# Kernel optimization log

Hardware: AMD Instinct MI355X
Metric: run time of the kernel (lower is better)

Reference implementation:

```python
import jax, jax.numpy as jnp
import numpy as np

B, S, D, H = 4, 2048, 1024, 16
Dh = D // H


def _layernorm(x, a, b):
    # torch.var default is unbiased (ddof=1)
    mu = jnp.mean(x, axis=-1, keepdims=True)
    sg = jnp.var(x, axis=-1, keepdims=True, ddof=1)
    return (x - mu) / jnp.sqrt(sg + 1e-08) * a + b


def setup_inputs() -> dict:
    key = jax.random.key(0)
    ks = jax.random.split(key, 16)
    s = 1.0 / np.sqrt(D)
    inp = {
        'q': jax.random.normal(ks[0], (B, S, D), jnp.float32),
        'k': jax.random.normal(ks[1], (B, S, D), jnp.float32),
        'v': jax.random.normal(ks[2], (B, S, D), jnp.float32),
        'g': jax.random.normal(ks[3], (B, S, D), jnp.float32),
        # causal mask: True = masked
        'm': jnp.triu(jnp.ones((S, S), jnp.bool_), k=1)[None, None],
        'Wq': jax.random.uniform(ks[4], (D, D), jnp.float32, -s, s),
        'bq': jnp.zeros((D,), jnp.float32),
        'Wk': jax.random.uniform(ks[5], (D, D), jnp.float32, -s, s),
        'bk': jnp.zeros((D,), jnp.float32),
        'Wv': jax.random.uniform(ks[6], (D, D), jnp.float32, -s, s),
        'bv': jnp.zeros((D,), jnp.float32),
        'Wg': jax.random.uniform(ks[7], (D, D), jnp.float32, -s, s),
        'bg': jnp.zeros((D,), jnp.float32),
        'ln_a': jnp.ones((D,), jnp.float32),
        'ln_b': jnp.zeros((D,), jnp.float32),
        'Wo': jax.random.uniform(ks[8], (D, D), jnp.float32, -s, s),
        'bo': jnp.zeros((D,), jnp.float32),
    }
    return inp


def reference(q, k, v, g, m, Wq, bq, Wk, bk, Wv, bv, Wg, bg, ln_a, ln_b, Wo, bo):
    qp = q @ Wq.T + bq
    kp = k @ Wk.T + bk
    vp = v @ Wv.T + bv
    gp = g @ Wg.T + bg
    # gating path: exact GELU (torch default), then custom LayerNorm (unbiased var)
    vp = jax.nn.gelu(vp, approximate=False)
    gp = jax.nn.gelu(gp, approximate=False)
    vp = _layernorm(vp, ln_a, ln_b)
    # [B,S,D] -> [B,H,S,Dh]
    qh = qp.reshape(B, S, H, Dh).transpose(0, 2, 1, 3)
    kh = kp.reshape(B, S, H, Dh).transpose(0, 2, 1, 3)
    vh = vp.reshape(B, S, H, Dh).transpose(0, 2, 1, 3)
    gh = gp.reshape(B, S, H, Dh).transpose(0, 2, 1, 3)
    a = jnp.einsum('bhqd,bhkd->bhqk', qh, kh) / jnp.sqrt(jnp.float32(Dh))
    a = jnp.where(m, -jnp.inf, a)
    a = jax.nn.softmax(a, axis=-1)
    # dropout = 0.0 (inference): no-op
    o = jnp.einsum('bhqk,bhkd->bhqd', a, vh)
    o = o * gh
    o = o.transpose(0, 2, 1, 3).reshape(B, S, D)
    o = o @ Wo.T + bo
    return (o, a)
```

## Files before the change

### kernel.cpp

```cpp
#include <hip/hip_runtime.h>
#include <hip/hip_bf16.h>
#include <cstdint>
#include <cstddef>

#define DEVINL static __device__ __forceinline__

typedef short bf16x8 __attribute__((ext_vector_type(8)));
typedef short s16x4  __attribute__((ext_vector_type(4)));
typedef float f32x4  __attribute__((ext_vector_type(4)));
typedef unsigned short u16;

static constexpr int Bb = 4, Ss = 2048, Dd = 1024, Hh = 16;
static constexpr int Mrows = Bb * Ss;
static constexpr int BHc = Bb * Hh;

DEVINL u16 f2bf(float f) {
    union { float f; uint32_t u; } v; v.f = f;
    uint32_t r = v.u + 0x7fffu + ((v.u >> 16) & 1u);
    return (u16)(r >> 16);
}
DEVINL float bf2f(u16 h) {
    union { uint32_t u; float f; } v; v.u = ((uint32_t)h) << 16;
    return v.f;
}
DEVINL uint32_t cvt_pk_bf16(float lo, float hi) {
    uint32_t r;
    asm("v_cvt_pk_bf16_f32 %0, %1, %2" : "=v"(r) : "v"(lo), "v"(hi));
    return r;
}
DEVINL float gelu_exact(float x) {
    return 0.5f * x * (1.0f + erff(x * 0.70710678118654752f));
}
DEVINL void gload16(const u16* gsrc, u16* ldsdst) {
    auto* g = reinterpret_cast<const __attribute__((address_space(1))) uint32_t*>(
        reinterpret_cast<uintptr_t>(gsrc));
    auto* l = reinterpret_cast<__attribute__((address_space(3))) uint32_t*>(
        reinterpret_cast<uintptr_t>(ldsdst));
    __builtin_amdgcn_global_load_lds(g, l, 16, 0, 0);
}

__global__ __launch_bounds__(256) void k_cvt_in(
    const float* __restrict__ s0, const float* __restrict__ s1,
    const float* __restrict__ s2, const float* __restrict__ s3,
    u16* __restrict__ d0, u16* __restrict__ d1,
    u16* __restrict__ d2, u16* __restrict__ d3, int n4) {
    int t = blockIdx.x * 256 + threadIdx.x;
    if (t >= n4) return;
    const float* s; u16* d;
    switch (blockIdx.y) {
        case 0: s = s0; d = d0; break;
        case 1: s = s1; d = d1; break;
        case 2: s = s2; d = d2; break;
        default: s = s3; d = d3; break;
    }
    float4 v = ((const float4*)s)[t];
    ushort4 o;
    o.x = f2bf(v.x); o.y = f2bf(v.y); o.z = f2bf(v.z); o.w = f2bf(v.w);
    ((ushort4*)d)[t] = o;
}

__global__ __launch_bounds__(256) void k_cvt_w(
    const float* __restrict__ s0, const float* __restrict__ s1,
    const float* __restrict__ s2, const float* __restrict__ s3,
    const float* __restrict__ s4,
    u16* __restrict__ d0, u16* __restrict__ d1, u16* __restrict__ d2,
    u16* __restrict__ d3, u16* __restrict__ d4, int n4) {
    int t = blockIdx.x * 256 + threadIdx.x;
    if (t >= n4) return;
    const float* s; u16* d;
    switch (blockIdx.y) {
        case 0: s = s0; d = d0; break;
        case 1: s = s1; d = d1; break;
        case 2: s = s2; d = d2; break;
        case 3: s = s3; d = d3; break;
        default: s = s4; d = d4; break;
    }
    float4 v = ((const float4*)s)[t];
    ushort4 o;
    o.x = f2bf(v.x); o.y = f2bf(v.y); o.z = f2bf(v.z); o.w = f2bf(v.w);
    ((ushort4*)d)[t] = o;
}

__global__ __launch_bounds__(256, 3) void k_proj(
    const u16* __restrict__ qb, const u16* __restrict__ kb,
    const u16* __restrict__ vb, const u16* __restrict__ gb,
    const u16* __restrict__ Wqb, const u16* __restrict__ Wkb,
    const u16* __restrict__ Wvb, const u16* __restrict__ Wgb,
    const float* __restrict__ bqp, const float* __restrict__ bkp,
    const float* __restrict__ bvp, const float* __restrict__ bgp,
    u16* __restrict__ qp, u16* __restrict__ kpo,
    float* __restrict__ vp, u16* __restrict__ ghb)
{
    __shared__ u16 As[2][128 * 32];
    __shared__ u16 Bs[2][128 * 32];
    const int tid = threadIdx.x, lane = tid & 63, w = tid >> 6;
    const int wm = w >> 1, wn = w & 1;
    const int g = lane >> 4, li = lane & 15;
    const int orig = blockIdx.x;
    const int lid = (orig & 7) * 256 + (orig >> 3);
    const int z = lid >> 9, rem = lid & 511;
    const int m0 = (rem >> 3) * 128, n0 = (rem & 7) * 128;

    const u16 *Ap, *Wp; const float* bias;
    switch (z) {
        case 0: Ap = qb; Wp = Wqb; bias = bqp; break;
        case 1: Ap = kb; Wp = Wkb; bias = bkp; break;
        case 2: Ap = vb; Wp = Wvb; bias = bvp; break;
        default: Ap = gb; Wp = Wgb; bias = bgp; break;
    }

    const int ch0 = (w * 2 + 0) * 64 + lane, ch1 = (w * 2 + 1) * 64 + lane;
    const int row0 = ch0 >> 2, cp0 = ch0 & 3, row1 = ch1 >> 2, cp1 = ch1 & 3;
    const size_t aoff0 = (size_t)(m0 + row0) * 1024 + ((cp0 ^ ((row0 >> 1) & 3)) << 3);
    const size_t aoff1 = (size_t)(m0 + row1) * 1024 + ((cp1 ^ ((row1 >> 1) & 3)) << 3);
    const size_t boff0 = (size_t)(n0 + row0) * 1024 + ((cp0 ^ ((row0 >> 1) & 3)) << 3);
    const size_t boff1 = (size_t)(n0 + row1) * 1024 + ((cp1 ^ ((row1 >> 1) & 3)) << 3);
    const int ldst0 = (w * 2 + 0) * 512, ldst1 = (w * 2 + 1) * 512;

    const f32x4 zero4 = {0.f, 0.f, 0.f, 0.f};
    f32x4 acc[4][4];
#pragma unroll
    for (int m = 0; m < 4; m++)
#pragma unroll
        for (int n = 0; n < 4; n++) acc[m][n] = zero4;

    gload16(Ap + aoff0,      &As[0][ldst0]);
    gload16(Ap + aoff1,      &As[0][ldst1]);
    gload16(Wp + boff0,      &Bs[0][ldst0]);
    gload16(Wp + boff1,      &Bs[0][ldst1]);
    gload16(Ap + aoff0 + 32, &As[1][ldst0]);
    gload16(Ap + aoff1 + 32, &As[1][ldst1]);
    gload16(Wp + boff0 + 32, &Bs[1][ldst0]);
    gload16(Wp + boff1 + 32, &Bs[1][ldst1]);
    asm volatile("s_waitcnt vmcnt(4)" ::: "memory");
    asm volatile("s_barrier" ::: "memory");

    for (int kt = 0; kt < 32; ++kt) {
        const int cur = kt & 1;
        bf16x8 af[4], bfr[4];
#pragma unroll
        for (int m = 0; m < 4; m++) {
            int row = wm * 64 + m * 16 + li;
            af[m] = *(const bf16x8*)&As[cur][row * 32 + ((g ^ ((row >> 1) & 3)) << 3)];
        }
#pragma unroll
        for (int n = 0; n < 4; n++) {
            int row = wn * 64 + n * 16 + li;
            bfr[n] = *(const bf16x8*)&Bs[cur][row * 32 + ((g ^ ((row >> 1) & 3)) << 3)];
        }
#pragma unroll
        for (int m = 0; m < 4; m++)
#pragma unroll
            for (int n = 0; n < 4; n++)
                acc[m][n] = __builtin_amdgcn_mfma_f32_16x16x32_bf16(af[m], bfr[n], acc[m][n], 0, 0, 0);
        asm volatile("s_barrier" ::: "memory");
        if (kt + 2 < 32) {
            const int k0n = (kt + 2) * 32;
            gload16(Ap + aoff0 + k0n, &As[cur][ldst0]);
            gload16(Ap + aoff1 + k0n, &As[cur][ldst1]);
            gload16(Wp + boff0 + k0n, &Bs[cur][ldst0]);
            gload16(Wp + boff1 + k0n, &Bs[cur][ldst1]);
            asm volatile("s_waitcnt vmcnt(4)" ::: "memory");
        } else {
            asm volatile("s_waitcnt vmcnt(0)" ::: "memory");
        }
        asm volatile("s_barrier" ::: "memory");
    }

#pragma unroll
    for (int m = 0; m < 4; m++) {
#pragma unroll
        for (int n = 0; n < 4; n++) {
            int col = n0 + wn * 64 + n * 16 + li;
            float bv = bias[col];
#pragma unroll
            for (int r = 0; r < 4; r++) {
                int row = m0 + wm * 64 + m * 16 + g * 4 + r;
                float v = acc[m][n][r] + bv;
                size_t idx = (size_t)row * 1024 + col;
                if (z == 0)      qp[idx]  = f2bf(v * 0.125f);
                else if (z == 1) kpo[idx] = f2bf(v);
                else if (z == 2) vp[idx]  = gelu_exact(v);
                else             ghb[idx] = f2bf(gelu_exact(v));
            }
        }
    }
}

__global__ __launch_bounds__(256, 3) void k_gemm_f(
    const u16* __restrict__ Ap, const u16* __restrict__ Wp,
    const float* __restrict__ bias, float* __restrict__ Cp)
{
    __shared__ u16 As[2][128 * 32];
    __shared__ u16 Bs[2][128 * 32];
    const int tid = threadIdx.x, lane = tid & 63, w = tid >> 6;
    const int wm = w >> 1, wn = w & 1;
    const int g = lane >> 4, li = lane & 15;
    const int orig = blockIdx.x;
    const int lid = (orig & 7) * 64 + (orig >> 3);
    const int m0 = (lid >> 3) * 128, n0 = (lid & 7) * 128;

    const int ch0 = (w * 2 + 0) * 64 + lane, ch1 = (w * 2 + 1) * 64 + lane;
    const int row0 = ch0 >> 2, cp0 = ch0 & 3, row1 = ch1 >> 2, cp1 = ch1 & 3;
    const size_t aoff0 = (size_t)(m0 + row0) * 1024 + ((cp0 ^ ((row0 >> 1) & 3)) << 3);
    const size_t aoff1 = (size_t)(m0 + row1) * 1024 + ((cp1 ^ ((row1 >> 1) & 3)) << 3);
    const size_t boff0 = (size_t)(n0 + row0) * 1024 + ((cp0 ^ ((row0 >> 1) & 3)) << 3);
    const size_t boff1 = (size_t)(n0 + row1) * 1024 + ((cp1 ^ ((row1 >> 1) & 3)) << 3);
    const int ldst0 = (w * 2 + 0) * 512, ldst1 = (w * 2 + 1) * 512;

    const f32x4 zero4 = {0.f, 0.f, 0.f, 0.f};
    f32x4 acc[4][4];
#pragma unroll
    for (int m = 0; m < 4; m++)
#pragma unroll
        for (int n = 0; n < 4; n++) acc[m][n] = zero4;

    gload16(Ap + aoff0,      &As[0][ldst0]);
    gload16(Ap + aoff1,      &As[0][ldst1]);
    gload16(Wp + boff0,      &Bs[0][ldst0]);
    gload16(Wp + boff1,      &Bs[0][ldst1]);
    gload16(Ap + aoff0 + 32, &As[1][ldst0]);
    gload16(Ap + aoff1 + 32, &As[1][ldst1]);
    gload16(Wp + boff0 + 32, &Bs[1][ldst0]);
    gload16(Wp + boff1 + 32, &Bs[1][ldst1]);
    asm volatile("s_waitcnt vmcnt(4)" ::: "memory");
    asm volatile("s_barrier" ::: "memory");

    for (int kt = 0; kt < 32; ++kt) {
        const int cur = kt & 1;
        bf16x8 af[4], bfr[4];
#pragma unroll
        for (int m = 0; m < 4; m++) {
            int row = wm * 64 + m * 16 + li;
            af[m] = *(const bf16x8*)&As[cur][row * 32 + ((g ^ ((row >> 1) & 3)) << 3)];
        }
#pragma unroll
        for (int n = 0; n < 4; n++) {
            int row = wn * 64 + n * 16 + li;
            bfr[n] = *(const bf16x8*)&Bs[cur][row * 32 + ((g ^ ((row >> 1) & 3)) << 3)];
        }
#pragma unroll
        for (int m = 0; m < 4; m++)
#pragma unroll
            for (int n = 0; n < 4; n++)
                acc[m][n] = __builtin_amdgcn_mfma_f32_16x16x32_bf16(af[m], bfr[n], acc[m][n], 0, 0, 0);
        asm volatile("s_barrier" ::: "memory");
        if (kt + 2 < 32) {
            const int k0n = (kt + 2) * 32;
            gload16(Ap + aoff0 + k0n, &As[cur][ldst0]);
            gload16(Ap + aoff1 + k0n, &As[cur][ldst1]);
            gload16(Wp + boff0 + k0n, &Bs[cur][ldst0]);
            gload16(Wp + boff1 + k0n, &Bs[cur][ldst1]);
            asm volatile("s_waitcnt vmcnt(4)" ::: "memory");
        } else {
            asm volatile("s_waitcnt vmcnt(0)" ::: "memory");
        }
        asm volatile("s_barrier" ::: "memory");
    }

#pragma unroll
    for (int m = 0; m < 4; m++) {
#pragma unroll
        for (int n = 0; n < 4; n++) {
            int col = n0 + wn * 64 + n * 16 + li;
            float bv = bias[col];
#pragma unroll
            for (int r = 0; r < 4; r++) {
                int row = m0 + wm * 64 + m * 16 + g * 4 + r;
                Cp[(size_t)row * 1024 + col] = acc[m][n][r] + bv;
            }
        }
    }
}

__global__ __launch_bounds__(256) void k_ln(const float* __restrict__ vp,
                                            const float* __restrict__ la,
                                            const float* __restrict__ lb,
                                            u16* __restrict__ vh) {
    int row = blockIdx.x;
    const float* x = vp + (size_t)row * 1024;
    int tid = threadIdx.x;
    float4 v = ((const float4*)x)[tid];
    float s = v.x + v.y + v.z + v.w;
    float s2 = v.x * v.x + v.y * v.y + v.z * v.z + v.w * v.w;
#pragma unroll
    for (int off = 1; off < 64; off <<= 1) {
        s  += __shfl_xor(s, off, 64);
        s2 += __shfl_xor(s2, off, 64);
    }
    __shared__ float red[8];
    int w = tid >> 6, lane = tid & 63;
    if (lane == 0) { red[w] = s; red[4 + w] = s2; }
    __syncthreads();
    s  = red[0] + red[1] + red[2] + red[3];
    s2 = red[4] + red[5] + red[6] + red[7];
    float mu = s * (1.0f / 1024.0f);
    float var = (s2 - 1024.0f * mu * mu) * (1.0f / 1023.0f);
    float rs = rsqrtf(var + 1e-8f);
    float4 a4 = ((const float4*)la)[tid];
    float4 b4 = ((const float4*)lb)[tid];
    ushort4 o;
    o.x = f2bf((v.x - mu) * rs * a4.x + b4.x);
    o.y = f2bf((v.y - mu) * rs * a4.y + b4.y);
    o.z = f2bf((v.z - mu) * rs * a4.z + b4.z);
    o.w = f2bf((v.w - mu) * rs * a4.w + b4.w);
    ((ushort4*)(vh + (size_t)row * 1024))[tid] = o;
}

__global__ __launch_bounds__(256) void k_transpose(const u16* __restrict__ vh,
                                                   u16* __restrict__ vhT) {
    int bh = blockIdx.y, b = bh >> 4, h = bh & 15, s0 = blockIdx.x * 64;
    __shared__ u16 t[64 * 96];
    int tid = threadIdx.x;
#pragma unroll
    for (int j = 0; j < 2; j++) {
        int u = j * 256 + tid;
        int r = u >> 3, c8 = u & 7;
        bf16x8 v = *(const bf16x8*)(vh + ((size_t)(b * 2048 + s0 + r) * 1024 + h * 64 + c8 * 8));
        *(bf16x8*)&t[r * 96 + c8 * 8] = v;
    }
    __syncthreads();
#pragma unroll
    for (int j = 0; j < 2; j++) {
        int u = j * 256 + tid;
        int d = u >> 3, s8 = u & 7;
        bf16x8 vv;
#pragma unroll
        for (int jj = 0; jj < 8; jj++) vv[jj] = (short)t[(s8 * 8 + jj) * 96 + d];
        *(bf16x8*)(vhT + ((size_t)(bh * 64 + d) * 2048 + s0 + s8 * 8)) = vv;
    }
}

__global__ __launch_bounds__(512) void k_attn(const u16* __restrict__ qp,
                                              const u16* __restrict__ kp,
                                              const u16* __restrict__ vhT,
                                              const u16* __restrict__ gh,
                                              float* __restrict__ aout,
                                              u16* __restrict__ gated) {
    __shared__ short Ps[8 * 16 * 128];
    const int tid = threadIdx.x, lane = tid & 63, w = tid >> 6;
    const int g = lane >> 4, li = lane & 15;
    const int orig = blockIdx.x;
    const int lid = (orig & 7) * 64 + (orig >> 3);
    const int bh = lid >> 3, i0 = lid & 7;
    const int b = bh >> 4, h = bh & 15;
    const u16* kbh = kp + ((size_t)(b * 2048) * 1024 + h * 64);
    const u16* vbh = vhT + (size_t)bh * 64 * 2048;
    const u16* ghb_base = gh + (size_t)(b * 2048) * 1024 + h * 64;
    float* arow = aout + (size_t)bh * 2048 * 2048;
    short* Pw = &Ps[w * 2048];
    const f32x4 zero4 = {0.f, 0.f, 0.f, 0.f};

    for (int half = 0; half < 2; ++half) {
        const int bx = half ? (15 - i0) : i0;
        const int q0 = bx * 128;
        const int qrow0 = q0 + w * 16;
        const int qrow = qrow0 + li;
        const u16* qbase = qp + ((size_t)(b * 2048 + qrow) * 1024 + h * 64 + g * 8);
        bf16x8 qa0 = *(const bf16x8*)qbase;
        bf16x8 qa1 = *(const bf16x8*)(qbase + 32);

        for (int kt = bx + 1; kt < 16; ++kt) {
            float* tbase = arow + (size_t)q0 * 2048 + kt * 128;
#pragma unroll
            for (int i = 0; i < 8; i++) {
                int u = i * 512 + tid;
                int row = u >> 5, cu = u & 31;
                __builtin_nontemporal_store(zero4, (f32x4*)(tbase + (size_t)row * 2048 + cu * 4));
            }
        }

        float l_run = 0.f;
        for (int kt = 0; kt <= bx; ++kt) {
            const int k0 = kt * 128;
            const bool full = (kt < bx);
#pragma unroll
            for (int n = 0; n < 8; n++) {
                int rb = k0 + n * 16 + li;
                const u16* krow = kbh + (size_t)rb * 1024 + g * 8;
                bf16x8 kb0 = *(const bf16x8*)krow;
                bf16x8 kb1 = *(const bf16x8*)(krow + 32);
                f32x4 c = zero4;
                c = __builtin_amdgcn_mfma_f32_16x16x32_bf16(kb0, qa0, c, 0, 0, 0);
                c = __builtin_amdgcn_mfma_f32_16x16x32_bf16(kb1, qa1, c, 0, 0, 0);
                if (full) {
#pragma unroll
                    for (int r = 0; r < 4; r++) l_run += __expf(c[r]);
                } else {
#pragma unroll
                    for (int r = 0; r < 4; r++) {
                        int col = k0 + n * 16 + g * 4 + r;
                        l_run += (col <= qrow) ? __expf(c[r]) : 0.0f;
                    }
                }
            }
        }
        l_run += __shfl_xor(l_run, 16, 64);
        l_run += __shfl_xor(l_run, 32, 64);
        const float linv = 1.0f / l_run;

        f32x4 oacc[4];
#pragma unroll
        for (int n = 0; n < 4; n++) oacc[n] = zero4;
        for (int kt = 0; kt <= bx; ++kt) {
            const int k0 = kt * 128;
            const bool full = (kt < bx);
#pragma unroll
            for (int n = 0; n < 8; n++) {
                int rb = k0 + n * 16 + li;
                const u16* krow = kbh + (size_t)rb * 1024 + g * 8;
                bf16x8 kb0 = *(const bf16x8*)krow;
                bf16x8 kb1 = *(const bf16x8*)(krow + 32);
                f32x4 c = zero4;
                c = __builtin_amdgcn_mfma_f32_16x16x32_bf16(kb0, qa0, c, 0, 0, 0);
                c = __builtin_amdgcn_mfma_f32_16x16x32_bf16(kb1, qa1, c, 0, 0, 0);
                if (full) {
#pragma unroll
                    for (int r = 0; r < 4; r++) c[r] = __expf(c[r]) * linv;
                } else {
#pragma unroll
                    for (int r = 0; r < 4; r++) {
                        int col = k0 + n * 16 + g * 4 + r;
                        c[r] = (col <= qrow) ? __expf(c[r]) * linv : 0.0f;
                    }
                }
                __builtin_nontemporal_store(c,
                    (f32x4*)(arow + (size_t)qrow * 2048 + k0 + n * 16 + g * 4));
                uint2 pk;
                pk.x = cvt_pk_bf16(c[0], c[1]);
                pk.y = cvt_pk_bf16(c[2], c[3]);
                int chunk = n * 2 + (g >> 1);
                *(uint2*)&Pw[li * 128 + ((chunk ^ (li & 7)) << 3) + (g & 1) * 4] = pk;
            }
#pragma unroll
            for (int ks = 0; ks < 4; ++ks) {
                int cl = ks * 4 + g;
                bf16x8 pa = *(const bf16x8*)&Pw[li * 128 + ((cl ^ (li & 7)) << 3)];
#pragma unroll
                for (int n = 0; n < 4; n++) {
                    int vr = n * 16 + li;
                    bf16x8 vb = *(const bf16x8*)(vbh + (size_t)vr * 2048 + k0 + cl * 8);
                    oacc[n] = __builtin_amdgcn_mfma_f32_16x16x32_bf16(pa, vb, oacc[n], 0, 0, 0);
                }
            }
        }

#pragma unroll
        for (int n = 0; n < 4; n++) {
            int d8 = n * 2 + (li >> 3), wi = li & 7;
#pragma unroll
            for (int r = 0; r < 4; r++) {
                int lr = g * 4 + r;
                Pw[lr * 64 + ((d8 ^ (lr & 7)) << 3) + wi] = (short)f2bf(oacc[n][r]);
            }
        }
#pragma unroll
        for (int it = 0; it < 2; ++it) {
            int lr = it * 8 + (lane >> 3);
            int c8 = lane & 7;
            int rowq = qrow0 + lr;
            bf16x8 ov = *(const bf16x8*)&Pw[lr * 64 + ((c8 ^ (lr & 7)) << 3)];
            bf16x8 gv = *(const bf16x8*)(ghb_base + (size_t)rowq * 1024 + c8 * 8);
            float p0 = bf2f((u16)ov[0]) * bf2f((u16)gv[0]);
            float p1 = bf2f((u16)ov[1]) * bf2f((u16)gv[1]);
            float p2 = bf2f((u16)ov[2]) * bf2f((u16)gv[2]);
            float p3 = bf2f((u16)ov[3]) * bf2f((u16)gv[3]);
            float p4 = bf2f((u16)ov[4]) * bf2f((u16)gv[4]);
            float p5 = bf2f((u16)ov[5]) * bf2f((u16)gv[5]);
            float p6 = bf2f((u16)ov[6]) * bf2f((u16)gv[6]);
            float p7 = bf2f((u16)ov[7]) * bf2f((u16)gv[7]);
            uint4 outv;
            outv.x = cvt_pk_bf16(p0, p1);
            outv.y = cvt_pk_bf16(p2, p3);
            outv.z = cvt_pk_bf16(p4, p5);
            outv.w = cvt_pk_bf16(p6, p7);
            *(uint4*)(gated + ((size_t)(b * 2048 + rowq)) * 1024 + h * 64 + c8 * 8) = outv;
        }
    }
}

extern "C" void kernel_launch(void* const* d_in, const int* in_sizes, int n_in,
                              void* d_out, int out_size, void* d_ws, size_t ws_size,
                              hipStream_t stream) {
    const float* q  = (const float*)d_in[0];
    const float* k  = (const float*)d_in[1];
    const float* v  = (const float*)d_in[2];
    const float* g  = (const float*)d_in[3];
    const float* Wq = (const float*)d_in[5];
    const float* bq = (const float*)d_in[6];
    const float* Wk = (const float*)d_in[7];
    const float* bk = (const float*)d_in[8];
    const float* Wv = (const float*)d_in[9];
    const float* bv = (const float*)d_in[10];
    const float* Wg = (const float*)d_in[11];
    const float* bg = (const float*)d_in[12];
    const float* ln_a = (const float*)d_in[13];
    const float* ln_b = (const float*)d_in[14];
    const float* Wo = (const float*)d_in[15];
    const float* bo = (const float*)d_in[16];

    float* o_out = (float*)d_out;
    float* a_out = o_out + (size_t)Mrows * Dd;

    u16* qp    = (u16*)d_ws;
    u16* kpb   = qp    + (size_t)Mrows * Dd;
    u16* vhT   = kpb   + (size_t)Mrows * Dd;
    u16* ghb   = vhT   + (size_t)Mrows * Dd;
    u16* gated = ghb   + (size_t)Mrows * Dd;
    u16* Wo_bf = gated + (size_t)Mrows * Dd;

    u16* Wq_bf = (u16*)a_out;
    u16* Wk_bf = Wq_bf + (size_t)Dd * Dd;
    u16* Wv_bf = Wk_bf + (size_t)Dd * Dd;
    u16* Wg_bf = Wv_bf + (size_t)Dd * Dd;
    u16* qb    = Wg_bf + (size_t)Dd * Dd;
    u16* kb2   = qb    + (size_t)Mrows * Dd;
    u16* vb    = kb2   + (size_t)Mrows * Dd;
    u16* gb    = vb    + (size_t)Mrows * Dd;
    float* vp  = (float*)(gb + (size_t)Mrows * Dd);
    u16* vh    = (u16*)(vp + (size_t)Mrows * Dd);

    {
        int n4w = Dd * Dd / 4;
        dim3 gw((n4w + 255) / 256, 5);
        k_cvt_w<<<gw, 256, 0, stream>>>(Wq, Wk, Wv, Wg, Wo,
                                        Wq_bf, Wk_bf, Wv_bf, Wg_bf, Wo_bf, n4w);
        int n4i = Mrows * Dd / 4;
        dim3 gi((n4i + 255) / 256, 4);
        k_cvt_in<<<gi, 256, 0, stream>>>(q, k, v, g, qb, kb2, vb, gb, n4i);
    }

    k_proj<<<2048, 256, 0, stream>>>(qb, kb2, vb, gb,
                                     Wq_bf, Wk_bf, Wv_bf, Wg_bf,
                                     bq, bk, bv, bg,
                                     qp, kpb, vp, ghb);

    k_ln<<<Mrows, 256, 0, stream>>>(vp, ln_a, ln_b, vh);

    dim3 gt(Ss / 64, BHc);
    k_transpose<<<gt, 256, 0, stream>>>(vh, vhT);

    k_attn<<<512, 512, 0, stream>>>(qp, kpb, vhT, ghb, a_out, gated);

    k_gemm_f<<<512, 256, 0, stream>>>(gated, Wo_bf, bo, o_out);
}
```

Measured before the change: 648.9 us.

## Fuse fp32-to-bf16 input conversion into projection GEMM A-tile loads

```diff
diff --git a/kernel.cpp b/kernel.cpp
--- a/kernel.cpp
+++ b/kernel.cpp
@@ -37,26 +37,6 @@
     auto* l = reinterpret_cast<__attribute__((address_space(3))) uint32_t*>(
         reinterpret_cast<uintptr_t>(ldsdst));
     __builtin_amdgcn_global_load_lds(g, l, 16, 0, 0);
-}
-
-__global__ __launch_bounds__(256) void k_cvt_in(
-    const float* __restrict__ s0, const float* __restrict__ s1,
-    const float* __restrict__ s2, const float* __restrict__ s3,
-    u16* __restrict__ d0, u16* __restrict__ d1,
-    u16* __restrict__ d2, u16* __restrict__ d3, int n4) {
-    int t = blockIdx.x * 256 + threadIdx.x;
-    if (t >= n4) return;
-    const float* s; u16* d;
-    switch (blockIdx.y) {
-        case 0: s = s0; d = d0; break;
-        case 1: s = s1; d = d1; break;
-        case 2: s = s2; d = d2; break;
-        default: s = s3; d = d3; break;
-    }
-    float4 v = ((const float4*)s)[t];
-    ushort4 o;
-    o.x = f2bf(v.x); o.y = f2bf(v.y); o.z = f2bf(v.z); o.w = f2bf(v.w);
-    ((ushort4*)d)[t] = o;
 }
 
 __global__ __launch_bounds__(256) void k_cvt_w(
@@ -82,8 +62,8 @@
 }
 
 __global__ __launch_bounds__(256, 3) void k_proj(
-    const u16* __restrict__ qb, const u16* __restrict__ kb,
-    const u16* __restrict__ vb, const u16* __restrict__ gb,
+    const float* __restrict__ qf, const float* __restrict__ kf,
+    const float* __restrict__ vf, const float* __restrict__ gf,
     const u16* __restrict__ Wqb, const u16* __restrict__ Wkb,
     const u16* __restrict__ Wvb, const u16* __restrict__ Wgb,
     const float* __restrict__ bqp, const float* __restrict__ bkp,
@@ -91,8 +71,8 @@
     u16* __restrict__ qp, u16* __restrict__ kpo,
     float* __restrict__ vp, u16* __restrict__ ghb)
 {
-    __shared__ u16 As[2][128 * 32];
-    __shared__ u16 Bs[2][128 * 32];
+    __shared__ u16 As[128 * 32];
+    __shared__ u16 Bs[128 * 32];
     const int tid = threadIdx.x, lane = tid & 63, w = tid >> 6;
     const int wm = w >> 1, wn = w & 1;
     const int g = lane >> 4, li = lane & 15;
@@ -101,21 +81,13 @@
     const int z = lid >> 9, rem = lid & 511;
     const int m0 = (rem >> 3) * 128, n0 = (rem & 7) * 128;
 
-    const u16 *Ap, *Wp; const float* bias;
+    const float* Af; const u16* Wp; const float* bias;
     switch (z) {
-        case 0: Ap = qb; Wp = Wqb; bias = bqp; break;
-        case 1: Ap = kb; Wp = Wkb; bias = bkp; break;
-        case 2: Ap = vb; Wp = Wvb; bias = bvp; break;
-        default: Ap = gb; Wp = Wgb; bias = bgp; break;
-    }
-
-    const int ch0 = (w * 2 + 0) * 64 + lane, ch1 = (w * 2 + 1) * 64 + lane;
-    const int row0 = ch0 >> 2, cp0 = ch0 & 3, row1 = ch1 >> 2, cp1 = ch1 & 3;
-    const size_t aoff0 = (size_t)(m0 + row0) * 1024 + ((cp0 ^ ((row0 >> 1) & 3)) << 3);
-    const size_t aoff1 = (size_t)(m0 + row1) * 1024 + ((cp1 ^ ((row1 >> 1) & 3)) << 3);
-    const size_t boff0 = (size_t)(n0 + row0) * 1024 + ((cp0 ^ ((row0 >> 1) & 3)) << 3);
-    const size_t boff1 = (size_t)(n0 + row1) * 1024 + ((cp1 ^ ((row1 >> 1) & 3)) << 3);
-    const int ldst0 = (w * 2 + 0) * 512, ldst1 = (w * 2 + 1) * 512;
+        case 0: Af = qf; Wp = Wqb; bias = bqp; break;
+        case 1: Af = kf; Wp = Wkb; bias = bkp; break;
+        case 2: Af = vf; Wp = Wvb; bias = bvp; break;
+        default: Af = gf; Wp = Wgb; bias = bgp; break;
+    }
 
     const f32x4 zero4 = {0.f, 0.f, 0.f, 0.f};
     f32x4 acc[4][4];
@@ -124,47 +96,44 @@
 #pragma unroll
         for (int n = 0; n < 4; n++) acc[m][n] = zero4;
 
-    gload16(Ap + aoff0,      &As[0][ldst0]);
-    gload16(Ap + aoff1,      &As[0][ldst1]);
-    gload16(Wp + boff0,      &Bs[0][ldst0]);
-    gload16(Wp + boff1,      &Bs[0][ldst1]);
-    gload16(Ap + aoff0 + 32, &As[1][ldst0]);
-    gload16(Ap + aoff1 + 32, &As[1][ldst1]);
-    gload16(Wp + boff0 + 32, &Bs[1][ldst0]);
-    gload16(Wp + boff1 + 32, &Bs[1][ldst1]);
-    asm volatile("s_waitcnt vmcnt(4)" ::: "memory");
-    asm volatile("s_barrier" ::: "memory");
-
-    for (int kt = 0; kt < 32; ++kt) {
-        const int cur = kt & 1;
+    for (int k0 = 0; k0 < 1024; k0 += 32) {
+        __syncthreads();
+#pragma unroll
+        for (int i = 0; i < 4; i++) {
+            int u = i * 256 + tid;
+            int row = u >> 3, c4 = u & 7;
+            float4 v = *(const float4*)(Af + (size_t)(m0 + row) * 1024 + k0 + c4 * 4);
+            uint2 o;
+            o.x = cvt_pk_bf16(v.x, v.y);
+            o.y = cvt_pk_bf16(v.z, v.w);
+            int off = row * 32 + ((((c4 >> 1) ^ ((row >> 1) & 3))) << 3) + ((c4 & 1) << 2);
+            *(uint2*)&As[off] = o;
+        }
+#pragma unroll
+        for (int i = 0; i < 2; i++) {
+            int chunk = (w * 2 + i) * 64 + lane;
+            int row = chunk >> 2, cp = chunk & 3;
+            gload16(Wp + (size_t)(n0 + row) * 1024 + k0 + ((cp ^ ((row >> 1) & 3)) << 3),
+                    &Bs[(w * 2 + i) * 512]);
+        }
+        __syncthreads();
+
         bf16x8 af[4], bfr[4];
 #pragma unroll
         for (int m = 0; m < 4; m++) {
             int row = wm * 64 + m * 16 + li;
-            af[m] = *(const bf16x8*)&As[cur][row * 32 + ((g ^ ((row >> 1) & 3)) << 3)];
+            af[m] = *(const bf16x8*)&As[row * 32 + ((g ^ ((row >> 1) & 3)) << 3)];
         }
 #pragma unroll
         for (int n = 0; n < 4; n++) {
             int row = wn * 64 + n * 16 + li;
-            bfr[n] = *(const bf16x8*)&Bs[cur][row * 32 + ((g ^ ((row >> 1) & 3)) << 3)];
+            bfr[n] = *(const bf16x8*)&Bs[row * 32 + ((g ^ ((row >> 1) & 3)) << 3)];
         }
 #pragma unroll
         for (int m = 0; m < 4; m++)
 #pragma unroll
             for (int n = 0; n < 4; n++)
                 acc[m][n] = __builtin_amdgcn_mfma_f32_16x16x32_bf16(af[m], bfr[n], acc[m][n], 0, 0, 0);
-        asm volatile("s_barrier" ::: "memory");
-        if (kt + 2 < 32) {
-            const int k0n = (kt + 2) * 32;
-            gload16(Ap + aoff0 + k0n, &As[cur][ldst0]);
-            gload16(Ap + aoff1 + k0n, &As[cur][ldst1]);
-            gload16(Wp + boff0 + k0n, &Bs[cur][ldst0]);
-            gload16(Wp + boff1 + k0n, &Bs[cur][ldst1]);
-            asm volatile("s_waitcnt vmcnt(4)" ::: "memory");
-        } else {
-            asm volatile("s_waitcnt vmcnt(0)" ::: "memory");
-        }
-        asm volatile("s_barrier" ::: "memory");
     }
 
 #pragma unroll
@@ -513,11 +482,7 @@
     u16* Wk_bf = Wq_bf + (size_t)Dd * Dd;
     u16* Wv_bf = Wk_bf + (size_t)Dd * Dd;
     u16* Wg_bf = Wv_bf + (size_t)Dd * Dd;
-    u16* qb    = Wg_bf + (size_t)Dd * Dd;
-    u16* kb2   = qb    + (size_t)Mrows * Dd;
-    u16* vb    = kb2   + (size_t)Mrows * Dd;
-    u16* gb    = vb    + (size_t)Mrows * Dd;
-    float* vp  = (float*)(gb + (size_t)Mrows * Dd);
+    float* vp  = (float*)(Wg_bf + (size_t)Dd * Dd);
     u16* vh    = (u16*)(vp + (size_t)Mrows * Dd);
 
     {
@@ -525,12 +490,9 @@
         dim3 gw((n4w + 255) / 256, 5);
         k_cvt_w<<<gw, 256, 0, stream>>>(Wq, Wk, Wv, Wg, Wo,
                                         Wq_bf, Wk_bf, Wv_bf, Wg_bf, Wo_bf, n4w);
-        int n4i = Mrows * Dd / 4;
-        dim3 gi((n4i + 255) / 256, 4);
-        k_cvt_in<<<gi, 256, 0, stream>>>(q, k, v, g, qb, kb2, vb, gb, n4i);
-    }
-
-    k_proj<<<2048, 256, 0, stream>>>(qb, kb2, vb, gb,
+    }
+
+    k_proj<<<2048, 256, 0, stream>>>(q, k, v, g,
                                      Wq_bf, Wk_bf, Wv_bf, Wg_bf,
                                      bq, bk, bv, bg,
                                      qp, kpb, vp, ghb);
```

After: 689.8 us. 6.3% more time.
